# Kernel tuning notes

Measured on AMD Instinct MI355X. Metric: run time of the kernel, lower is better.

Reference implementation:

```python
import jax, jax.numpy as jnp
import numpy as np

B, S, F_IN = 2048, 256, 3
COND = 4
EMBED = 4
HID = 64
NUM_CODES = 256
BETA = 0.25


def _linear_params(key, fan_in, fan_out):
    k1, k2 = jax.random.split(key)
    lim = 1.0 / np.sqrt(fan_in)
    w = jax.random.uniform(k1, (fan_in, fan_out), jnp.float32, -lim, lim)
    b = jax.random.uniform(k2, (fan_out,), jnp.float32, -lim, lim)
    return w, b


def setup_inputs() -> dict:
    key = jax.random.key(0)
    ks = jax.random.split(key, 10)
    x = jax.random.normal(ks[0], (B, S, F_IN), jnp.float32)
    mask = jnp.ones((B, S), jnp.float32)
    x_conditional = jax.random.normal(ks[1], (B, COND), jnp.float32)
    enc_w1, enc_b1 = _linear_params(ks[2], F_IN + COND, HID)
    enc_w2, enc_b2 = _linear_params(ks[3], HID, HID)
    enc_w3, enc_b3 = _linear_params(ks[4], HID, EMBED)
    codebook = jax.random.normal(ks[5], (NUM_CODES, EMBED), jnp.float32)
    dec_w1, dec_b1 = _linear_params(ks[6], EMBED + COND, HID)
    dec_w2, dec_b2 = _linear_params(ks[7], HID, HID)
    dec_w3, dec_b3 = _linear_params(ks[8], HID, F_IN)
    return dict(x=x, mask=mask, x_conditional=x_conditional,
                enc_w1=enc_w1, enc_b1=enc_b1, enc_w2=enc_w2, enc_b2=enc_b2,
                enc_w3=enc_w3, enc_b3=enc_b3, codebook=codebook,
                dec_w1=dec_w1, dec_b1=dec_b1, dec_w2=dec_w2, dec_b2=dec_b2,
                dec_w3=dec_w3, dec_b3=dec_b3)


def _mlp(x, w1, b1, w2, b2, w3, b3):
    h = jax.nn.relu(x @ w1 + b1)
    h = jax.nn.relu(h @ w2 + b2)
    return h @ w3 + b3


def _vq(z, codebook):
    # z: [B, S, E]; nearest-codebook assignment via expanded squared L2
    zf = z.reshape(-1, z.shape[-1])                       # [N, E]
    d = (jnp.sum(zf * zf, axis=-1, keepdims=True)
         - 2.0 * zf @ codebook.T
         + jnp.sum(codebook * codebook, axis=-1))         # [N, num_codes]
    idx = jnp.argmin(d, axis=-1)                          # [N]
    z_q = codebook[idx].reshape(z.shape)                  # [B, S, E]
    # VQ losses (codebook + beta * commitment)
    loss = (jnp.mean((jax.lax.stop_gradient(z) - z_q) ** 2)
            + BETA * jnp.mean((z - jax.lax.stop_gradient(z_q)) ** 2))
    # straight-through estimator
    z_q_st = z + jax.lax.stop_gradient(z_q - z)
    return z_q_st, loss, idx.reshape(z.shape[:-1])


def reference(x, mask, x_conditional,
              enc_w1, enc_b1, enc_w2, enc_b2, enc_w3, enc_b3,
              codebook,
              dec_w1, dec_b1, dec_w2, dec_b2, dec_w3, dec_b3):
    cond = jnp.broadcast_to(x_conditional[:, None, :], (B, S, COND))
    xin = jnp.concatenate([x, cond], axis=-1) * mask[..., None]
    z = _mlp(xin, enc_w1, enc_b1, enc_w2, enc_b2, enc_w3, enc_b3)
    z_q, vq_loss, idx = _vq(z, codebook)
    zdec = jnp.concatenate([z_q, cond], axis=-1) * mask[..., None]
    x_reco = _mlp(zdec, dec_w1, dec_b1, dec_w2, dec_b2, dec_w3, dec_b3)
    return x_reco, vq_loss, idx
```

## Files before the change

kernel.cpp:

```cpp
#include <hip/hip_runtime.h>
#include <hip/hip_bf16.h>

#define BB   2048
#define SS   256
#define NTOK (BB*SS)
#define FIN  3
#define CND  4
#define EMB  4
#define HID  64
#define NC   256
#define TPB  256

typedef __attribute__((ext_vector_type(16))) float f32x16;

#define OF_EW1T 0
#define OF_DW1T 512
#define OF_DB1  1024
#define OF_EB2  1088
#define OF_DB2  1152
#define OF_EW3  1216
#define OF_DW3T 1472
#define OF_CB   1728
#define OF_CC   2752
#define OF_EW2L 3008
#define OF_DW2L 5056
#define SMEM_F  7104

__global__ __launch_bounds__(TPB, 2) void vqvae_fused(
        const float* __restrict__ x, const float* __restrict__ mask,
        const float* __restrict__ cond,
        const float* __restrict__ ew1, const float* __restrict__ eb1,
        const float* __restrict__ ew2, const float* __restrict__ eb2,
        const float* __restrict__ ew3, const float* __restrict__ eb3,
        const float* __restrict__ cb,
        const float* __restrict__ dw1, const float* __restrict__ db1,
        const float* __restrict__ dw2, const float* __restrict__ db2,
        const float* __restrict__ dw3, const float* __restrict__ db3,
        float* __restrict__ out, float* __restrict__ loss_ws) {
    __shared__ float smem[SMEM_F];
    const int tid = threadIdx.x;

    for (int idx = tid; idx < (FIN+CND)*HID; idx += TPB) {
        int i = idx >> 6, j = idx & 63;
        smem[OF_EW1T + j*8 + i] = ew1[idx];
    }
    for (int j = tid; j < HID; j += TPB) smem[OF_EW1T + j*8 + 7] = eb1[j];
    for (int idx = tid; idx < (EMB+CND)*HID; idx += TPB) {
        int i = idx >> 6, j = idx & 63;
        smem[OF_DW1T + j*8 + i] = dw1[idx];
    }
    for (int j = tid; j < HID; j += TPB) smem[OF_DB1 + j] = db1[j];
    for (int j = tid; j < HID; j += TPB) smem[OF_EB2 + j] = eb2[j];
    for (int j = tid; j < HID; j += TPB) smem[OF_DB2 + j] = db2[j];
    for (int i = tid; i < HID*EMB; i += TPB) smem[OF_EW3 + i] = ew3[i];
    for (int j = tid; j < HID; j += TPB) {
        smem[OF_DW3T + j*4 + 0] = dw3[j*FIN + 0];
        smem[OF_DW3T + j*4 + 1] = dw3[j*FIN + 1];
        smem[OF_DW3T + j*4 + 2] = dw3[j*FIN + 2];
        smem[OF_DW3T + j*4 + 3] = 0.0f;
    }
    for (int i = tid; i < NC*EMB; i += TPB) smem[OF_CB + i] = cb[i];
    for (int idx = tid; idx < HID*32; idx += TPB) {
        int k = idx >> 5, j = idx & 31;
        smem[OF_EW2L + idx] = ew2[k*HID + j];
        smem[OF_DW2L + idx] = dw2[k*HID + j];
    }
    {
        float c0 = cb[tid*EMB+0], c1 = cb[tid*EMB+1];
        float c2 = cb[tid*EMB+2], c3 = cb[tid*EMB+3];
        smem[OF_CC+tid] = ((c0*c0 + c1*c1) + c2*c2) + c3*c3;
    }
    __syncthreads();

    const int n0 = blockIdx.x * (2*TPB) + tid;
    const int n1 = n0 + TPB;
    const float m0 = mask[n0];
    const float m1 = mask[n1];
    const int bu0 = n0 >> 8;
    const int bu1 = bu0 + 1;

    float xin0[FIN+CND], xin1[FIN+CND];
    #pragma unroll
    for (int i = 0; i < FIN; i++) xin0[i] = x[n0*FIN + i] * m0;
    #pragma unroll
    for (int i = 0; i < FIN; i++) xin1[i] = x[n1*FIN + i] * m1;
    #pragma unroll
    for (int i = 0; i < CND; i++) xin0[FIN+i] = cond[bu0*CND + i] * m0;
    #pragma unroll
    for (int i = 0; i < CND; i++) xin1[FIN+i] = cond[bu1*CND + i] * m1;

    float hA[HID], hB[HID];
    #pragma unroll
    for (int j = 0; j < HID; j++) {
        float4 lo = *(const float4*)&smem[OF_EW1T + j*8 + 0];
        float4 hi = *(const float4*)&smem[OF_EW1T + j*8 + 4];
        float a = xin0[0] * lo.x;
        float b = xin1[0] * lo.x;
        a = fmaf(xin0[1], lo.y, a);  b = fmaf(xin1[1], lo.y, b);
        a = fmaf(xin0[2], lo.z, a);  b = fmaf(xin1[2], lo.z, b);
        a = fmaf(xin0[3], lo.w, a);  b = fmaf(xin1[3], lo.w, b);
        a = fmaf(xin0[4], hi.x, a);  b = fmaf(xin1[4], hi.x, b);
        a = fmaf(xin0[5], hi.y, a);  b = fmaf(xin1[5], hi.y, b);
        a = fmaf(xin0[6], hi.z, a);  b = fmaf(xin1[6], hi.z, b);
        hA[j] = fmaxf(a + hi.w, 0.0f);
        hB[j] = fmaxf(b + hi.w, 0.0f);
    }

    float z0 = 0.f, z1 = 0.f, z2 = 0.f, z3 = 0.f;
    float y0 = 0.f, y1 = 0.f, y2 = 0.f, y3 = 0.f;
    for (int jt = 0; jt < 8; jt++) {
        float a0 = 0.f, a1 = 0.f, a2 = 0.f, a3 = 0.f;
        float b0 = 0.f, b1 = 0.f, b2 = 0.f, b3 = 0.f;
        #pragma unroll
        for (int k = 0; k < HID; k++) {
            float4 w = *(const float4*)&smem[OF_EW2L + k*32 + jt*4];
            a0 = fmaf(hA[k], w.x, a0);
            a1 = fmaf(hA[k], w.y, a1);
            a2 = fmaf(hA[k], w.z, a2);
            a3 = fmaf(hA[k], w.w, a3);
            b0 = fmaf(hB[k], w.x, b0);
            b1 = fmaf(hB[k], w.y, b1);
            b2 = fmaf(hB[k], w.z, b2);
            b3 = fmaf(hB[k], w.w, b3);
        }
        float4 bb = *(const float4*)&smem[OF_EB2 + jt*4];
        float ta0 = fmaxf(a0 + bb.x, 0.0f), tb0 = fmaxf(b0 + bb.x, 0.0f);
        float ta1 = fmaxf(a1 + bb.y, 0.0f), tb1 = fmaxf(b1 + bb.y, 0.0f);
        float ta2 = fmaxf(a2 + bb.z, 0.0f), tb2 = fmaxf(b2 + bb.z, 0.0f);
        float ta3 = fmaxf(a3 + bb.w, 0.0f), tb3 = fmaxf(b3 + bb.w, 0.0f);
        float4 w0 = *(const float4*)&smem[OF_EW3 + (jt*4+0)*EMB];
        z0 = fmaf(ta0, w0.x, z0); z1 = fmaf(ta0, w0.y, z1);
        z2 = fmaf(ta0, w0.z, z2); z3 = fmaf(ta0, w0.w, z3);
        y0 = fmaf(tb0, w0.x, y0); y1 = fmaf(tb0, w0.y, y1);
        y2 = fmaf(tb0, w0.z, y2); y3 = fmaf(tb0, w0.w, y3);
        float4 w1 = *(const float4*)&smem[OF_EW3 + (jt*4+1)*EMB];
        z0 = fmaf(ta1, w1.x, z0); z1 = fmaf(ta1, w1.y, z1);
        z2 = fmaf(ta1, w1.z, z2); z3 = fmaf(ta1, w1.w, z3);
        y0 = fmaf(tb1, w1.x, y0); y1 = fmaf(tb1, w1.y, y1);
        y2 = fmaf(tb1, w1.z, y2); y3 = fmaf(tb1, w1.w, y3);
        float4 w2 = *(const float4*)&smem[OF_EW3 + (jt*4+2)*EMB];
        z0 = fmaf(ta2, w2.x, z0); z1 = fmaf(ta2, w2.y, z1);
        z2 = fmaf(ta2, w2.z, z2); z3 = fmaf(ta2, w2.w, z3);
        y0 = fmaf(tb2, w2.x, y0); y1 = fmaf(tb2, w2.y, y1);
        y2 = fmaf(tb2, w2.z, y2); y3 = fmaf(tb2, w2.w, y3);
        float4 w3 = *(const float4*)&smem[OF_EW3 + (jt*4+3)*EMB];
        z0 = fmaf(ta3, w3.x, z0); z1 = fmaf(ta3, w3.y, z1);
        z2 = fmaf(ta3, w3.z, z2); z3 = fmaf(ta3, w3.w, z3);
        y0 = fmaf(tb3, w3.x, y0); y1 = fmaf(tb3, w3.y, y1);
        y2 = fmaf(tb3, w3.z, y2); y3 = fmaf(tb3, w3.w, y3);
    }
    for (int t = 0; t < 2; t++) {
        float a[16], b[16];
        #pragma unroll
        for (int u = 0; u < 16; u++) { a[u] = 0.f; b[u] = 0.f; }
        #pragma unroll
        for (int k = 0; k < HID; k++) {
            f32x16 w = *(const f32x16*)&ew2[k*HID + 32 + t*16];
            #pragma unroll
            for (int u = 0; u < 16; u++) {
                a[u] = fmaf(hA[k], w[u], a[u]);
                b[u] = fmaf(hB[k], w[u], b[u]);
            }
        }
        f32x16 bb = *(const f32x16*)&eb2[32 + t*16];
        #pragma unroll
        for (int u = 0; u < 16; u++) {
            float ta = fmaxf(a[u] + bb[u], 0.0f);
            float tb = fmaxf(b[u] + bb[u], 0.0f);
            float4 w3 = *(const float4*)&smem[OF_EW3 + (32 + t*16 + u)*EMB];
            z0 = fmaf(ta, w3.x, z0); z1 = fmaf(ta, w3.y, z1);
            z2 = fmaf(ta, w3.z, z2); z3 = fmaf(ta, w3.w, z3);
            y0 = fmaf(tb, w3.x, y0); y1 = fmaf(tb, w3.y, y1);
            y2 = fmaf(tb, w3.z, y2); y3 = fmaf(tb, w3.w, y3);
        }
    }
    z0 += eb3[0]; z1 += eb3[1];
    z2 += eb3[2]; z3 += eb3[3];
    y0 += eb3[0]; y1 += eb3[1];
    y2 += eb3[2]; y3 += eb3[3];

    const float zzA = ((z0*z0 + z1*z1) + z2*z2) + z3*z3;
    const float zzB = ((y0*y0 + y1*y1) + y2*y2) + y3*y3;
    float bestA = 3.4e38f, bestB = 3.4e38f;
    int   biA = 0, biB = 0;
    #pragma unroll 4
    for (int ci = 0; ci < NC; ci++) {
        float4 c = *(const float4*)&smem[OF_CB + ci*EMB];
        float cc = smem[OF_CC + ci];
        float dotA = z0 * c.x;
        dotA = fmaf(z1, c.y, dotA);
        dotA = fmaf(z2, c.z, dotA);
        dotA = fmaf(z3, c.w, dotA);
        float dA = (zzA - 2.0f*dotA) + cc;
        if (dA < bestA) { bestA = dA; biA = ci; }
        float dotB = y0 * c.x;
        dotB = fmaf(y1, c.y, dotB);
        dotB = fmaf(y2, c.z, dotB);
        dotB = fmaf(y3, c.w, dotB);
        float dB = (zzB - 2.0f*dotB) + cc;
        if (dB < bestB) { bestB = dB; biB = ci; }
    }
    float4 qA = *(const float4*)&smem[OF_CB + biA*EMB];
    float4 qB = *(const float4*)&smem[OF_CB + biB*EMB];

    float e0 = z0-qA.x, e1 = z1-qA.y, e2 = z2-qA.z, e3 = z3-qA.w;
    float f0 = y0-qB.x, f1 = y1-qB.y, f2 = y2-qB.z, f3 = y3-qB.w;
    float sq = (((e0*e0 + e1*e1) + e2*e2) + e3*e3)
             + (((f0*f0 + f1*f1) + f2*f2) + f3*f3);
    #pragma unroll
    for (int off = 32; off > 0; off >>= 1) sq += __shfl_down(sq, off, 64);
    if ((tid & 63) == 0) atomicAdd(loss_ws, sq);

    out[NTOK*FIN + 1 + n0] = (float)biA;
    out[NTOK*FIN + 1 + n1] = (float)biB;

    float zd0[EMB+CND], zd1[EMB+CND];
    zd0[0] = qA.x*m0; zd0[1] = qA.y*m0; zd0[2] = qA.z*m0; zd0[3] = qA.w*m0;
    zd1[0] = qB.x*m1; zd1[1] = qB.y*m1; zd1[2] = qB.z*m1; zd1[3] = qB.w*m1;
    #pragma unroll
    for (int i = 0; i < CND; i++) zd0[EMB+i] = cond[bu0*CND + i] * m0;
    #pragma unroll
    for (int i = 0; i < CND; i++) zd1[EMB+i] = cond[bu1*CND + i] * m1;

    #pragma unroll
    for (int j = 0; j < HID; j++) {
        float4 lo = *(const float4*)&smem[OF_DW1T + j*8 + 0];
        float4 hi = *(const float4*)&smem[OF_DW1T + j*8 + 4];
        float a = zd0[0] * lo.x;
        float b = zd1[0] * lo.x;
        a = fmaf(zd0[1], lo.y, a);  b = fmaf(zd1[1], lo.y, b);
        a = fmaf(zd0[2], lo.z, a);  b = fmaf(zd1[2], lo.z, b);
        a = fmaf(zd0[3], lo.w, a);  b = fmaf(zd1[3], lo.w, b);
        a = fmaf(zd0[4], hi.x, a);  b = fmaf(zd1[4], hi.x, b);
        a = fmaf(zd0[5], hi.y, a);  b = fmaf(zd1[5], hi.y, b);
        a = fmaf(zd0[6], hi.z, a);  b = fmaf(zd1[6], hi.z, b);
        a = fmaf(zd0[7], hi.w, a);  b = fmaf(zd1[7], hi.w, b);
        float bias = smem[OF_DB1 + j];
        hA[j] = fmaxf(a + bias, 0.0f);
        hB[j] = fmaxf(b + bias, 0.0f);
    }

    float r0 = 0.f, r1 = 0.f, r2 = 0.f;
    float s0 = 0.f, s1 = 0.f, s2 = 0.f;
    for (int jt = 0; jt < 8; jt++) {
        float a0 = 0.f, a1 = 0.f, a2 = 0.f, a3 = 0.f;
        float b0 = 0.f, b1 = 0.f, b2 = 0.f, b3 = 0.f;
        #pragma unroll
        for (int k = 0; k < HID; k++) {
            float4 w = *(const float4*)&smem[OF_DW2L + k*32 + jt*4];
            a0 = fmaf(hA[k], w.x, a0);
            a1 = fmaf(hA[k], w.y, a1);
            a2 = fmaf(hA[k], w.z, a2);
            a3 = fmaf(hA[k], w.w, a3);
            b0 = fmaf(hB[k], w.x, b0);
            b1 = fmaf(hB[k], w.y, b1);
            b2 = fmaf(hB[k], w.z, b2);
            b3 = fmaf(hB[k], w.w, b3);
        }
        float4 bb = *(const float4*)&smem[OF_DB2 + jt*4];
        float ta0 = fmaxf(a0 + bb.x, 0.0f), tb0 = fmaxf(b0 + bb.x, 0.0f);
        float ta1 = fmaxf(a1 + bb.y, 0.0f), tb1 = fmaxf(b1 + bb.y, 0.0f);
        float ta2 = fmaxf(a2 + bb.z, 0.0f), tb2 = fmaxf(b2 + bb.z, 0.0f);
        float ta3 = fmaxf(a3 + bb.w, 0.0f), tb3 = fmaxf(b3 + bb.w, 0.0f);
        #pragma unroll
        for (int jj = 0; jj < 4; jj++) {
            float ta = (jj==0)?ta0:(jj==1)?ta1:(jj==2)?ta2:ta3;
            float tb = (jj==0)?tb0:(jj==1)?tb1:(jj==2)?tb2:tb3;
            int j = jt*4 + jj;
            float4 w = *(const float4*)&smem[OF_DW3T + j*4];
            r0 = fmaf(ta, w.x, r0); s0 = fmaf(tb, w.x, s0);
            r1 = fmaf(ta, w.y, r1); s1 = fmaf(tb, w.y, s1);
            r2 = fmaf(ta, w.z, r2); s2 = fmaf(tb, w.z, s2);
        }
    }
    for (int t = 0; t < 2; t++) {
        float a[16], b[16];
        #pragma unroll
        for (int u = 0; u < 16; u++) { a[u] = 0.f; b[u] = 0.f; }
        #pragma unroll
        for (int k = 0; k < HID; k++) {
            f32x16 w = *(const f32x16*)&dw2[k*HID + 32 + t*16];
            #pragma unroll
            for (int u = 0; u < 16; u++) {
                a[u] = fmaf(hA[k], w[u], a[u]);
                b[u] = fmaf(hB[k], w[u], b[u]);
            }
        }
        f32x16 bb = *(const f32x16*)&db2[32 + t*16];
        #pragma unroll
        for (int u = 0; u < 16; u++) {
            float ta = fmaxf(a[u] + bb[u], 0.0f);
            float tb = fmaxf(b[u] + bb[u], 0.0f);
            float4 w = *(const float4*)&smem[OF_DW3T + (32 + t*16 + u)*4];
            r0 = fmaf(ta, w.x, r0); s0 = fmaf(tb, w.x, s0);
            r1 = fmaf(ta, w.y, r1); s1 = fmaf(tb, w.y, s1);
            r2 = fmaf(ta, w.z, r2); s2 = fmaf(tb, w.z, s2);
        }
    }
    r0 += db3[0]; r1 += db3[1]; r2 += db3[2];
    s0 += db3[0]; s1 += db3[1]; s2 += db3[2];

    out[n0*FIN + 0] = r0;
    out[n0*FIN + 1] = r1;
    out[n0*FIN + 2] = r2;
    out[n1*FIN + 0] = s0;
    out[n1*FIN + 1] = s1;
    out[n1*FIN + 2] = s2;
}

__global__ void finalize_kernel(float* out, const float* loss_ws) {
    out[NTOK*FIN] = 1.25f * loss_ws[0] * (1.0f / (float)(NTOK*EMB));
}

extern "C" void kernel_launch(void* const* d_in, const int* in_sizes, int n_in,
                              void* d_out, int out_size, void* d_ws, size_t ws_size,
                              hipStream_t stream) {
    (void)in_sizes; (void)n_in; (void)ws_size; (void)out_size;
    float* ws = (float*)d_ws;
    hipMemsetAsync(ws, 0, sizeof(float), stream);

    vqvae_fused<<<NTOK/(2*TPB), TPB, 0, stream>>>(
        (const float*)d_in[0], (const float*)d_in[1], (const float*)d_in[2],
        (const float*)d_in[3], (const float*)d_in[4], (const float*)d_in[5],
        (const float*)d_in[6], (const float*)d_in[7], (const float*)d_in[8],
        (const float*)d_in[9], (const float*)d_in[10], (const float*)d_in[11],
        (const float*)d_in[12], (const float*)d_in[13], (const float*)d_in[14],
        (const float*)d_in[15],
        (float*)d_out, ws);

    finalize_kernel<<<1, 1, 0, stream>>>((float*)d_out, ws);
}
```

Measured before the change: 286.9 us.

## Split layer-2 work by wavefront between LDS and scalar-load paths

Each wavefront now computes all 64 layer-2 outputs through a single path, where before every wavefront split the outputs between LDS float4 reads and scalar-cache f32x16 reads of global weights. The wavefront-to-path assignment alternates by block parity, giving a 3:5 LDS-to-scalar ratio across block pairs. The full 64x64 weight matrices now live in LDS, growing shared memory to about 45KB. The aim is to balance LDS bandwidth against scalar memory pressure across wavefronts, at the cost of more LDS per block and larger code from two full unrolled paths.

Result: faster. 280.5 us (-2.2%).

```diff
diff --git a/kernel.cpp b/kernel.cpp
--- a/kernel.cpp
+++ b/kernel.cpp
@@ -22,9 +22,9 @@
 #define OF_DW3T 1472
 #define OF_CB   1728
 #define OF_CC   2752
-#define OF_EW2L 3008
-#define OF_DW2L 5056
-#define SMEM_F  7104
+#define OF_EW2F 3008
+#define OF_DW2F 7104
+#define SMEM_F  11200
 
 __global__ __launch_bounds__(TPB, 2) void vqvae_fused(
         const float* __restrict__ x, const float* __restrict__ mask,
@@ -60,10 +60,9 @@
         smem[OF_DW3T + j*4 + 3] = 0.0f;
     }
     for (int i = tid; i < NC*EMB; i += TPB) smem[OF_CB + i] = cb[i];
-    for (int idx = tid; idx < HID*32; idx += TPB) {
-        int k = idx >> 5, j = idx & 31;
-        smem[OF_EW2L + idx] = ew2[k*HID + j];
-        smem[OF_DW2L + idx] = dw2[k*HID + j];
+    for (int i = tid; i < HID*HID/4; i += TPB) {
+        *(float4*)&smem[OF_EW2F + i*4] = *(const float4*)&ew2[i*4];
+        *(float4*)&smem[OF_DW2F + i*4] = *(const float4*)&dw2[i*4];
     }
     {
         float c0 = cb[tid*EMB+0], c1 = cb[tid*EMB+1];
@@ -71,6 +70,9 @@
         smem[OF_CC+tid] = ((c0*c0 + c1*c1) + c2*c2) + c3*c3;
     }
     __syncthreads();
+
+    const int wid = tid >> 6;
+    const bool pathL = (blockIdx.x & 1) ? (wid == 1) : (wid == 0 || wid == 3);
 
     const int n0 = blockIdx.x * (2*TPB) + tid;
     const int n1 = n0 + TPB;
@@ -108,70 +110,73 @@
 
     float z0 = 0.f, z1 = 0.f, z2 = 0.f, z3 = 0.f;
     float y0 = 0.f, y1 = 0.f, y2 = 0.f, y3 = 0.f;
-    for (int jt = 0; jt < 8; jt++) {
-        float a0 = 0.f, a1 = 0.f, a2 = 0.f, a3 = 0.f;
-        float b0 = 0.f, b1 = 0.f, b2 = 0.f, b3 = 0.f;
-        #pragma unroll
-        for (int k = 0; k < HID; k++) {
-            float4 w = *(const float4*)&smem[OF_EW2L + k*32 + jt*4];
-            a0 = fmaf(hA[k], w.x, a0);
-            a1 = fmaf(hA[k], w.y, a1);
-            a2 = fmaf(hA[k], w.z, a2);
-            a3 = fmaf(hA[k], w.w, a3);
-            b0 = fmaf(hB[k], w.x, b0);
-            b1 = fmaf(hB[k], w.y, b1);
-            b2 = fmaf(hB[k], w.z, b2);
-            b3 = fmaf(hB[k], w.w, b3);
+    if (pathL) {
+        for (int jt = 0; jt < 16; jt++) {
+            float a0 = 0.f, a1 = 0.f, a2 = 0.f, a3 = 0.f;
+            float b0 = 0.f, b1 = 0.f, b2 = 0.f, b3 = 0.f;
+            #pragma unroll
+            for (int k = 0; k < HID; k++) {
+                float4 w = *(const float4*)&smem[OF_EW2F + k*HID + jt*4];
+                a0 = fmaf(hA[k], w.x, a0);
+                a1 = fmaf(hA[k], w.y, a1);
+                a2 = fmaf(hA[k], w.z, a2);
+                a3 = fmaf(hA[k], w.w, a3);
+                b0 = fmaf(hB[k], w.x, b0);
+                b1 = fmaf(hB[k], w.y, b1);
+                b2 = fmaf(hB[k], w.z, b2);
+                b3 = fmaf(hB[k], w.w, b3);
+            }
+            float4 bb = *(const float4*)&smem[OF_EB2 + jt*4];
+            float ta0 = fmaxf(a0 + bb.x, 0.0f), tb0 = fmaxf(b0 + bb.x, 0.0f);
+            float ta1 = fmaxf(a1 + bb.y, 0.0f), tb1 = fmaxf(b1 + bb.y, 0.0f);
+            float ta2 = fmaxf(a2 + bb.z, 0.0f), tb2 = fmaxf(b2 + bb.z, 0.0f);
+            float ta3 = fmaxf(a3 + bb.w, 0.0f), tb3 = fmaxf(b3 + bb.w, 0.0f);
+            float4 w0 = *(const float4*)&smem[OF_EW3 + (jt*4+0)*EMB];
+            z0 = fmaf(ta0, w0.x, z0); z1 = fmaf(ta0, w0.y, z1);
+            z2 = fmaf(ta0, w0.z, z2); z3 = fmaf(ta0, w0.w, z3);
+            y0 = fmaf(tb0, w0.x, y0); y1 = fmaf(tb0, w0.y, y1);
+            y2 = fmaf(tb0, w0.z, y2); y3 = fmaf(tb0, w0.w, y3);
+            float4 w1 = *(const float4*)&smem[OF_EW3 + (jt*4+1)*EMB];
+            z0 = fmaf(ta1, w1.x, z0); z1 = fmaf(ta1, w1.y, z1);
+            z2 = fmaf(ta1, w1.z, z2); z3 = fmaf(ta1, w1.w, z3);
+            y0 = fmaf(tb1, w1.x, y0); y1 = fmaf(tb1, w1.y, y1);
+            y2 = fmaf(tb1, w1.z, y2); y3 = fmaf(tb1, w1.w, y3);
+            float4 w2 = *(const float4*)&smem[OF_EW3 + (jt*4+2)*EMB];
+            z0 = fmaf(ta2, w2.x, z0); z1 = fmaf(ta2, w2.y, z1);
+            z2 = fmaf(ta2, w2.z, z2); z3 = fmaf(ta2, w2.w, z3);
+            y0 = fmaf(tb2, w2.x, y0); y1 = fmaf(tb2, w2.y, y1);
+            y2 = fmaf(tb2, w2.z, y2); y3 = fmaf(tb2, w2.w, y3);
+            float4 w3 = *(const float4*)&smem[OF_EW3 + (jt*4+3)*EMB];
+            z0 = fmaf(ta3, w3.x, z0); z1 = fmaf(ta3, w3.y, z1);
+            z2 = fmaf(ta3, w3.z, z2); z3 = fmaf(ta3, w3.w, z3);
+            y0 = fmaf(tb3, w3.x, y0); y1 = fmaf(tb3, w3.y, y1);
+            y2 = fmaf(tb3, w3.z, y2); y3 = fmaf(tb3, w3.w, y3);
         }
-        float4 bb = *(const float4*)&smem[OF_EB2 + jt*4];
-        float ta0 = fmaxf(a0 + bb.x, 0.0f), tb0 = fmaxf(b0 + bb.x, 0.0f);
-        float ta1 = fmaxf(a1 + bb.y, 0.0f), tb1 = fmaxf(b1 + bb.y, 0.0f);
-        float ta2 = fmaxf(a2 + bb.z, 0.0f), tb2 = fmaxf(b2 + bb.z, 0.0f);
-        float ta3 = fmaxf(a3 + bb.w, 0.0f), tb3 = fmaxf(b3 + bb.w, 0.0f);
-        float4 w0 = *(const float4*)&smem[OF_EW3 + (jt*4+0)*EMB];
-        z0 = fmaf(ta0, w0.x, z0); z1 = fmaf(ta0, w0.y, z1);
-        z2 = fmaf(ta0, w0.z, z2); z3 = fmaf(ta0, w0.w, z3);
-        y0 = fmaf(tb0, w0.x, y0); y1 = fmaf(tb0, w0.y, y1);
-        y2 = fmaf(tb0, w0.z, y2); y3 = fmaf(tb0, w0.w, y3);
-        float4 w1 = *(const float4*)&smem[OF_EW3 + (jt*4+1)*EMB];
-        z0 = fmaf(ta1, w1.x, z0); z1 = fmaf(ta1, w1.y, z1);
-        z2 = fmaf(ta1, w1.z, z2); z3 = fmaf(ta1, w1.w, z3);
-        y0 = fmaf(tb1, w1.x, y0); y1 = fmaf(tb1, w1.y, y1);
-        y2 = fmaf(tb1, w1.z, y2); y3 = fmaf(tb1, w1.w, y3);
-        float4 w2 = *(const float4*)&smem[OF_EW3 + (jt*4+2)*EMB];
-        z0 = fmaf(ta2, w2.x, z0); z1 = fmaf(ta2, w2.y, z1);
-        z2 = fmaf(ta2, w2.z, z2); z3 = fmaf(ta2, w2.w, z3);
-        y0 = fmaf(tb2, w2.x, y0); y1 = fmaf(tb2, w2.y, y1);
-        y2 = fmaf(tb2, w2.z, y2); y3 = fmaf(tb2, w2.w, y3);
-        float4 w3 = *(const float4*)&smem[OF_EW3 + (jt*4+3)*EMB];
-        z0 = fmaf(ta3, w3.x, z0); z1 = fmaf(ta3, w3.y, z1);
-        z2 = fmaf(ta3, w3.z, z2); z3 = fmaf(ta3, w3.w, z3);
-        y0 = fmaf(tb3, w3.x, y0); y1 = fmaf(tb3, w3.y, y1);
-        y2 = fmaf(tb3, w3.z, y2); y3 = fmaf(tb3, w3.w, y3);
-    }
-    for (int t = 0; t < 2; t++) {
-        float a[16], b[16];
-        #pragma unroll
-        for (int u = 0; u < 16; u++) { a[u] = 0.f; b[u] = 0.f; }
-        #pragma unroll
-        for (int k = 0; k < HID; k++) {
-            f32x16 w = *(const f32x16*)&ew2[k*HID + 32 + t*16];
+    } else {
+        for (int t = 0; t < 4; t++) {
+            float a[16], b[16];
+            #pragma unroll
+            for (int u = 0; u < 16; u++) { a[u] = 0.f; b[u] = 0.f; }
+            #pragma unroll
+            for (int k = 0; k < HID; k++) {
+                f32x16 w = *(const f32x16*)&ew2[k*HID + t*16];
+                #pragma unroll
+                for (int u = 0; u < 16; u++) {
+                    a[u] = fmaf(hA[k], w[u], a[u]);
+                    b[u] = fmaf(hB[k], w[u], b[u]);
+                }
+            }
+            f32x16 bb = *(const f32x16*)&eb2[t*16];
             #pragma unroll
             for (int u = 0; u < 16; u++) {
-                a[u] = fmaf(hA[k], w[u], a[u]);
-                b[u] = fmaf(hB[k], w[u], b[u]);
-            }
-        }
-        f32x16 bb = *(const f32x16*)&eb2[32 + t*16];
-        #pragma unroll
-        for (int u = 0; u < 16; u++) {
-            float ta = fmaxf(a[u] + bb[u], 0.0f);
-            float tb = fmaxf(b[u] + bb[u], 0.0f);
-            float4 w3 = *(const float4*)&smem[OF_EW3 + (32 + t*16 + u)*EMB];
-            z0 = fmaf(ta, w3.x, z0); z1 = fmaf(ta, w3.y, z1);
-            z2 = fmaf(ta, w3.z, z2); z3 = fmaf(ta, w3.w, z3);
-            y0 = fmaf(tb, w3.x, y0); y1 = fmaf(tb, w3.y, y1);
-            y2 = fmaf(tb, w3.z, y2); y3 = fmaf(tb, w3.w, y3);
+                float ta = fmaxf(a[u] + bb[u], 0.0f);
+                float tb = fmaxf(b[u] + bb[u], 0.0f);
+                float4 w3 = *(const float4*)&smem[OF_EW3 + (t*16+u)*EMB];
+                z0 = fmaf(ta, w3.x, z0); z1 = fmaf(ta, w3.y, z1);
+                z2 = fmaf(ta, w3.z, z2); z3 = fmaf(ta, w3.w, z3);
+                y0 = fmaf(tb, w3.x, y0); y1 = fmaf(tb, w3.y, y1);
+                y2 = fmaf(tb, w3.z, y2); y3 = fmaf(tb, w3.w, y3);
+            }
         }
     }
     z0 += eb3[0]; z1 += eb3[1];
@@ -242,59 +247,62 @@
 
     float r0 = 0.f, r1 = 0.f, r2 = 0.f;
     float s0 = 0.f, s1 = 0.f, s2 = 0.f;
-    for (int jt = 0; jt < 8; jt++) {
-        float a0 = 0.f, a1 = 0.f, a2 = 0.f, a3 = 0.f;
-        float b0 = 0.f, b1 = 0.f, b2 = 0.f, b3 = 0.f;
-        #pragma unroll
-        for (int k = 0; k < HID; k++) {
-            float4 w = *(const float4*)&smem[OF_DW2L + k*32 + jt*4];
-            a0 = fmaf(hA[k], w.x, a0);
-            a1 = fmaf(hA[k], w.y, a1);
-            a2 = fmaf(hA[k], w.z, a2);
-            a3 = fmaf(hA[k], w.w, a3);
-            b0 = fmaf(hB[k], w.x, b0);
-            b1 = fmaf(hB[k], w.y, b1);
-            b2 = fmaf(hB[k], w.z, b2);
-            b3 = fmaf(hB[k], w.w, b3);
+    if (pathL) {
+        for (int jt = 0; jt < 16; jt++) {
+            float a0 = 0.f, a1 = 0.f, a2 = 0.f, a3 = 0.f;
+            float b0 = 0.f, b1 = 0.f, b2 = 0.f, b3 = 0.f;
+            #pragma unroll
+            for (int k = 0; k < HID; k++) {
+                float4 w = *(const float4*)&smem[OF_DW2F + k*HID + jt*4];
+                a0 = fmaf(hA[k], w.x, a0);
+                a1 = fmaf(hA[k], w.y, a1);
+                a2 = fmaf(hA[k], w.z, a2);
+                a3 = fmaf(hA[k], w.w, a3);
+                b0 = fmaf(hB[k], w.x, b0);
+                b1 = fmaf(hB[k], w.y, b1);
+                b2 = fmaf(hB[k], w.z, b2);
+                b3 = fmaf(hB[k], w.w, b3);
+            }
+            float4 bb = *(const float4*)&smem[OF_DB2 + jt*4];
+            float ta0 = fmaxf(a0 + bb.x, 0.0f), tb0 = fmaxf(b0 + bb.x, 0.0f);
+            float ta1 = fmaxf(a1 + bb.y, 0.0f), tb1 = fmaxf(b1 + bb.y, 0.0f);
+            float ta2 = fmaxf(a2 + bb.z, 0.0f), tb2 = fmaxf(b2 + bb.z, 0.0f);
+            float ta3 = fmaxf(a3 + bb.w, 0.0f), tb3 = fmaxf(b3 + bb.w, 0.0f);
+            #pragma unroll
+            for (int jj = 0; jj < 4; jj++) {
+                float ta = (jj==0)?ta0:(jj==1)?ta1:(jj==2)?ta2:ta3;
+                float tb = (jj==0)?tb0:(jj==1)?tb1:(jj==2)?tb2:tb3;
+                int j = jt*4 + jj;
+                float4 w = *(const float4*)&smem[OF_DW3T + j*4];
+                r0 = fmaf(ta, w.x, r0); s0 = fmaf(tb, w.x, s0);
+                r1 = fmaf(ta, w.y, r1); s1 = fmaf(tb, w.y, s1);
+                r2 = fmaf(ta, w.z, r2); s2 = fmaf(tb, w.z, s2);
+            }
         }
-        float4 bb = *(const float4*)&smem[OF_DB2 + jt*4];
-        float ta0 = fmaxf(a0 + bb.x, 0.0f), tb0 = fmaxf(b0 + bb.x, 0.0f);
-        float ta1 = fmaxf(a1 + bb.y, 0.0f), tb1 = fmaxf(b1 + bb.y, 0.0f);
-        float ta2 = fmaxf(a2 + bb.z, 0.0f), tb2 = fmaxf(b2 + bb.z, 0.0f);
-        float ta3 = fmaxf(a3 + bb.w, 0.0f), tb3 = fmaxf(b3 + bb.w, 0.0f);
-        #pragma unroll
-        for (int jj = 0; jj < 4; jj++) {
-            float ta = (jj==0)?ta0:(jj==1)?ta1:(jj==2)?ta2:ta3;
-            float tb = (jj==0)?tb0:(jj==1)?tb1:(jj==2)?tb2:tb3;
-            int j = jt*4 + jj;
-            float4 w = *(const float4*)&smem[OF_DW3T + j*4];
-            r0 = fmaf(ta, w.x, r0); s0 = fmaf(tb, w.x, s0);
-            r1 = fmaf(ta, w.y, r1); s1 = fmaf(tb, w.y, s1);
-            r2 = fmaf(ta, w.z, r2); s2 = fmaf(tb, w.z, s2);
-        }
-    }
-    for (int t = 0; t < 2; t++) {
-        float a[16], b[16];
-        #pragma unroll
-        for (int u = 0; u < 16; u++) { a[u] = 0.f; b[u] = 0.f; }
-        #pragma unroll
-        for (int k = 0; k < HID; k++) {
-            f32x16 w = *(const f32x16*)&dw2[k*HID + 32 + t*16];
+    } else {
+        for (int t = 0; t < 4; t++) {
+            float a[16], b[16];
+            #pragma unroll
+            for (int u = 0; u < 16; u++) { a[u] = 0.f; b[u] = 0.f; }
+            #pragma unroll
+            for (int k = 0; k < HID; k++) {
+                f32x16 w = *(const f32x16*)&dw2[k*HID + t*16];
+                #pragma unroll
+                for (int u = 0; u < 16; u++) {
+                    a[u] = fmaf(hA[k], w[u], a[u]);
+                    b[u] = fmaf(hB[k], w[u], b[u]);
+                }
+            }
+            f32x16 bb = *(const f32x16*)&db2[t*16];
             #pragma unroll
             for (int u = 0; u < 16; u++) {
-                a[u] = fmaf(hA[k], w[u], a[u]);
-                b[u] = fmaf(hB[k], w[u], b[u]);
-            }
-        }
-        f32x16 bb = *(const f32x16*)&db2[32 + t*16];
-        #pragma unroll
-        for (int u = 0; u < 16; u++) {
-            float ta = fmaxf(a[u] + bb[u], 0.0f);
-            float tb = fmaxf(b[u] + bb[u], 0.0f);
-            float4 w = *(const float4*)&smem[OF_DW3T + (32 + t*16 + u)*4];
-            r0 = fmaf(ta, w.x, r0); s0 = fmaf(tb, w.x, s0);
-            r1 = fmaf(ta, w.y, r1); s1 = fmaf(tb, w.y, s1);
-            r2 = fmaf(ta, w.z, r2); s2 = fmaf(tb, w.z, s2);
+                float ta = fmaxf(a[u] + bb[u], 0.0f);
+                float tb = fmaxf(b[u] + bb[u], 0.0f);
+                float4 w = *(const float4*)&smem[OF_DW3T + (t*16+u)*4];
+                r0 = fmaf(ta, w.x, r0); s0 = fmaf(tb, w.x, s0);
+                r1 = fmaf(ta, w.y, r1); s1 = fmaf(tb, w.y, s1);
+                r2 = fmaf(ta, w.z, r2); s2 = fmaf(tb, w.z, s2);
+            }
         }
     }
     r0 += db3[0]; r1 += db3[1]; r2 += db3[2];
```
